# Performance work log

Hardware: AMD Instinct MI355X
Metric: run time of the kernel (lower is better)

## Reference

```python
import jax, jax.numpy as jnp
import numpy as np

D, H, W = 20, 18, 18      # f_dim = (20, 72//4, 72//4); depth == feature_ch
PI = 3.14159              # constant used in the torch module


def make_grid():
    # matches make_coordinate_grid_3d: normalized coords in [-1, 1]
    x = 2.0 * jnp.arange(W, dtype=jnp.float32) / (W - 1) - 1.0
    y = 2.0 * jnp.arange(H, dtype=jnp.float32) / (H - 1) - 1.0
    z = 2.0 * jnp.arange(D, dtype=jnp.float32) / (D - 1) - 1.0
    xx = jnp.broadcast_to(x[None, None, :], (D, H, W))
    yy = jnp.broadcast_to(y[None, :, None], (D, H, W))
    zz = jnp.broadcast_to(z[:, None, None], (D, H, W))
    grid_xy = jnp.stack([xx, yy], axis=-1)   # (D,H,W,2), order (x, y)
    return grid_xy, zz


def trilinear_sample(vol, grid):
    # vol: (D,H,W); grid: (D,H,W,3) with (x,y,z) in [-1,1]
    # F.grid_sample defaults: mode='bilinear' (trilinear), padding='zeros', align_corners=False
    ix = ((grid[..., 0] + 1.0) * W - 1.0) * 0.5
    iy = ((grid[..., 1] + 1.0) * H - 1.0) * 0.5
    iz = ((grid[..., 2] + 1.0) * D - 1.0) * 0.5
    x0, y0, z0 = jnp.floor(ix), jnp.floor(iy), jnp.floor(iz)
    wx, wy, wz = ix - x0, iy - y0, iz - z0
    vflat = vol.reshape(-1)
    out = jnp.zeros_like(ix)
    for cz in (0, 1):
        for cy in (0, 1):
            for cx in (0, 1):
                xi = x0 + cx
                yi = y0 + cy
                zi = z0 + cz
                w = ((wx if cx else 1.0 - wx)
                     * (wy if cy else 1.0 - wy)
                     * (wz if cz else 1.0 - wz))
                valid = ((xi >= 0) & (xi < W) & (yi >= 0) & (yi < H)
                         & (zi >= 0) & (zi < D))
                xi_c = jnp.clip(xi, 0, W - 1).astype(jnp.int32)
                yi_c = jnp.clip(yi, 0, H - 1).astype(jnp.int32)
                zi_c = jnp.clip(zi, 0, D - 1).astype(jnp.int32)
                idx = (zi_c * H + yi_c) * W + xi_c
                out = out + jnp.where(valid, w * vflat[idx], 0.0)
    return out


def setup_inputs() -> dict:
    key = jax.random.key(0)
    ks = jax.random.split(key, 10)
    B, P, F = 4096, 256, 20
    s = 0.05
    return {
        "feature_map": jax.random.normal(ks[0], (B, F, H, W), jnp.float32),
        "para_code": jax.random.normal(ks[1], (B, P), jnp.float32),
        "W1": jax.random.normal(ks[2], (P, P), jnp.float32) * s,
        "b1": jax.random.normal(ks[3], (P,), jnp.float32) * s,
        "Ws": jax.random.normal(ks[4], (P, F), jnp.float32) * s,
        "bs": jax.random.normal(ks[5], (F,), jnp.float32) * s,
        "Wr": jax.random.normal(ks[6], (P, F), jnp.float32) * s,
        "br": jax.random.normal(ks[7], (F,), jnp.float32) * s,
        "Wt": jax.random.normal(ks[8], (P, 2 * F), jnp.float32) * s,
        "bt": jax.random.normal(ks[9], (2 * F,), jnp.float32) * s,
    }


def reference(feature_map, para_code, W1, b1, Ws, bs, Wr, br, Wt, bt):
    B, F = feature_map.shape[0], feature_map.shape[1]  # F == D == 20
    grid_xy, grid_z = make_grid()
    h = jax.nn.relu(para_code @ W1 + b1)                     # commn_linear
    scale = jax.nn.sigmoid(h @ Ws + bs) * 2.0                # (B,F)
    angle = jnp.tanh(h @ Wr + br) * PI                       # (B,F)
    trans = jnp.tanh(h @ Wt + bt).reshape(B, F, 2)           # (B,F,2)
    c, s = jnp.cos(angle), jnp.sin(angle)
    rot = jnp.stack([jnp.stack([c, -s], -1),
                     jnp.stack([s, c], -1)], -2)             # (B,F,2,2)
    g = grid_xy.reshape(F, H * W, 2)                          # depth == feature_ch
    # per-channel affine: rotate, scale, translate each grid point
    tg = jnp.einsum('bfij,fpj->bfpi', rot, g)                 # (B,F,HW,2)
    tg = tg * scale[:, :, None, None] + trans[:, :, None, :]
    full_grid = jnp.concatenate(
        [tg.reshape(B, F, H, W, 2),
         jnp.broadcast_to(grid_z, (B, F, H, W))[..., None]], axis=-1)
    return jax.vmap(trilinear_sample)(feature_map, full_grid)
```

## Files before the change

### kernel.cpp

```cpp
#include <hip/hip_runtime.h>

#define PI_F 3.14159f

__global__ __launch_bounds__(256) void params_kernel(
    const float* __restrict__ pc, const float* __restrict__ W1, const float* __restrict__ b1,
    const float* __restrict__ Ws, const float* __restrict__ bs,
    const float* __restrict__ Wr, const float* __restrict__ br,
    const float* __restrict__ Wt, const float* __restrict__ bt,
    float* __restrict__ params)
{
    __shared__ float hbuf[4][260];
    __shared__ float raw[4][80];

    const int t    = threadIdx.x;
    const int lane = t & 63;
    const int b0   = blockIdx.x * 4;

    float pval[4][4];
    #pragma unroll
    for (int g = 0; g < 4; ++g)
        #pragma unroll
        for (int c = 0; c < 4; ++c)
            pval[g][c] = pc[(size_t)(b0 + g) * 256 + c * 64 + lane];

    float acc[4];
    #pragma unroll
    for (int g = 0; g < 4; ++g) acc[g] = b1[t];

    #pragma unroll
    for (int c = 0; c < 4; ++c) {
        for (int kk = 0; kk < 64; ++kk) {
            float w = W1[(c * 64 + kk) * 256 + t];
            #pragma unroll
            for (int g = 0; g < 4; ++g) {
                float pk = __int_as_float(
                    __builtin_amdgcn_readlane(__float_as_int(pval[g][c]), kk));
                acc[g] = fmaf(pk, w, acc[g]);
            }
        }
    }
    #pragma unroll
    for (int g = 0; g < 4; ++g) hbuf[g][t] = fmaxf(acc[g], 0.0f);
    __syncthreads();

    for (int task = t; task < 320; task += 256) {
        int g   = task / 80;
        int col = task - g * 80;
        const float* Wcol;
        float bias;
        int stride;
        if (col < 20)      { Wcol = Ws + col;        bias = bs[col];      stride = 20; }
        else if (col < 40) { Wcol = Wr + (col - 20); bias = br[col - 20]; stride = 20; }
        else               { Wcol = Wt + (col - 40); bias = bt[col - 40]; stride = 40; }
        const float4* h4 = (const float4*)hbuf[g];
        float a = bias;
        for (int k4 = 0; k4 < 64; ++k4) {
            float4 h = h4[k4];
            int k = k4 * 4;
            a = fmaf(h.x, Wcol[k * stride], a);
            a = fmaf(h.y, Wcol[(k + 1) * stride], a);
            a = fmaf(h.z, Wcol[(k + 2) * stride], a);
            a = fmaf(h.w, Wcol[(k + 3) * stride], a);
        }
        raw[g][col] = a;
    }
    __syncthreads();

    for (int task = t; task < 80; task += 256) {
        int g = task / 20;
        int f = task - g * 20;
        float sc  = 2.0f / (1.0f + expf(-raw[g][f]));
        float ang = PI_F * tanhf(raw[g][20 + f]);
        float tx  = tanhf(raw[g][40 + 2 * f]);
        float ty  = tanhf(raw[g][40 + 2 * f + 1]);
        float c = cosf(ang), s = sinf(ang);
        float* o = params + ((size_t)(b0 + g) * 20 + f) * 8;
        o[0] = 9.0f * sc * c;  o[1] = -9.0f * sc * s;  o[2] = fmaf(9.0f, tx, 9.5f);
        o[3] = 9.0f * sc * s;  o[4] =  9.0f * sc * c;  o[5] = fmaf(9.0f, ty, 9.5f);
        o[6] = 0.0f;           o[7] = 0.0f;
    }
}

__global__ __launch_bounds__(256, 8) void sample_kernel(
    const float* __restrict__ fmap, const float* __restrict__ params,
    float* __restrict__ out)
{
    __shared__ __align__(16) float lds[4][424];

    const int t    = threadIdx.x;
    const int lane = t & 63;
    const int w    = t >> 6;
    const int bid  = blockIdx.x;
    const int b    = bid / 5;
    const int c    = (bid - b * 5) * 4 + w;
    float* wv = lds[w];

    #pragma unroll
    for (int r = 0; r < 2; ++r) {
        int i = r * 64 + lane;
        if (i < 100) {
            int idx;
            if (i < 20)      idx = i;
            else if (i < 40) idx = 380 + (i - 20);
            else if (i < 76) {
                int q = i - 40;
                int y = 1 + (q < 18 ? q : q - 18);
                idx = y * 20 + (q < 18 ? 0 : 19);
            } else idx = 400 + (i - 76);
            wv[idx] = 0.0f;
        }
    }

    const float izf = (40.0f * (float)c - 19.0f) * (1.0f / 38.0f);
    const float fz0 = floorf(izf);
    const int   z0  = (int)fz0;
    const float wzB = izf - fz0;
    const bool  v0  = (z0 >= 0);
    const bool  v1  = (z0 + 1 <= 19);
    const float ew0 = v0 ? (1.0f - wzB) : 0.0f;
    const float ew1 = v1 ? wzB : 0.0f;
    const float* fb = fmap + (size_t)b * 6480;
    const float* s0 = fb + (v0 ? z0 : 0) * 324;
    const float* s1 = fb + (v1 ? z0 + 1 : 19) * 324;

    #pragma unroll
    for (int it = 0; it < 6; ++it) {
        int i = it * 64 + lane;
        if (i < 324) {
            float a  = s0[i];
            float bb = s1[i];
            int y = i / 18, x = i - y * 18;
            wv[(y + 1) * 20 + (x + 1)] = fmaf(a, ew0, bb * ew1);
        }
    }

    const float* pp = params + ((size_t)b * 20 + c) * 8;
    const float4 pA = *(const float4*)pp;
    const float2 pB = *(const float2*)(pp + 4);

    float* ob = out + (size_t)b * 6480 + c * 324;
    #pragma unroll
    for (int it = 0; it < 6; ++it) {
        int i = it * 64 + lane;
        if (i < 324) {
            int y = i / 18, x = i - y * 18;
            float X = (float)x * (2.0f / 17.0f) - 1.0f;
            float Y = (float)y * (2.0f / 17.0f) - 1.0f;
            float ix = fmaf(pA.x, X, fmaf(pA.y, Y, pA.z));
            float iy = fmaf(pA.w, X, fmaf(pB.x, Y, pB.y));
            ix = fminf(fmaxf(ix, 0.0f), 19.0f);
            iy = fminf(fmaxf(iy, 0.0f), 19.0f);
            float fx = floorf(ix), fy = floorf(iy);
            float u1 = ix - fx, vv = iy - fy;
            const float* s = wv + ((int)fy * 20 + (int)fx);
            float t00 = s[0], t01 = s[1], t10 = s[20], t11 = s[21];
            float u0 = 1.0f - u1, vc = 1.0f - vv;
            float r = fmaf(fmaf(t01, u1, t00 * u0), vc,
                           fmaf(t11, u1, t10 * u0) * vv);
            ob[i] = r;
        }
    }
}

extern "C" void kernel_launch(void* const* d_in, const int* in_sizes, int n_in,
                              void* d_out, int out_size, void* d_ws, size_t ws_size,
                              hipStream_t stream)
{
    const float* fmap = (const float*)d_in[0];
    const float* pc   = (const float*)d_in[1];
    const float* W1   = (const float*)d_in[2];
    const float* b1   = (const float*)d_in[3];
    const float* Ws   = (const float*)d_in[4];
    const float* bs   = (const float*)d_in[5];
    const float* Wr   = (const float*)d_in[6];
    const float* br   = (const float*)d_in[7];
    const float* Wt   = (const float*)d_in[8];
    const float* bt   = (const float*)d_in[9];
    float* out    = (float*)d_out;
    float* params = (float*)d_ws;

    const int B = in_sizes[0] / (20 * 18 * 18);

    params_kernel<<<B / 4, 256, 0, stream>>>(pc, W1, b1, Ws, bs, Wr, br, Wt, bt, params);
    sample_kernel<<<B * 5, 256, 0, stream>>>(fmap, params, out);
}
```

Measured before the change: 242.6 us.

## Batch 8 rows per params block and vectorize sampling with float2 and stride-21 LDS

The params kernel now handles 8 batch rows per block instead of 4, so each W1 load is reused across twice as many rows, and a couple of loops are unrolled. The sample kernel loads and stores float2 pairs, with each thread handling two adjacent pixels. The padded LDS tile row stride changes from 20 to 21, with the zero-border initialization rewritten to match. The params load is also hoisted above the tile fill. This trades more registers per thread and half as many params blocks for fewer memory instructions and better W1 reuse.

```diff
diff --git a/kernel.cpp b/kernel.cpp
--- a/kernel.cpp
+++ b/kernel.cpp
@@ -9,30 +9,31 @@
     const float* __restrict__ Wt, const float* __restrict__ bt,
     float* __restrict__ params)
 {
-    __shared__ float hbuf[4][260];
-    __shared__ float raw[4][80];
+    __shared__ float hbuf[8][260];
+    __shared__ float raw[8][80];
 
     const int t    = threadIdx.x;
     const int lane = t & 63;
-    const int b0   = blockIdx.x * 4;
-
-    float pval[4][4];
-    #pragma unroll
-    for (int g = 0; g < 4; ++g)
+    const int b0   = blockIdx.x * 8;
+
+    float pval[8][4];
+    #pragma unroll
+    for (int g = 0; g < 8; ++g)
         #pragma unroll
         for (int c = 0; c < 4; ++c)
             pval[g][c] = pc[(size_t)(b0 + g) * 256 + c * 64 + lane];
 
-    float acc[4];
-    #pragma unroll
-    for (int g = 0; g < 4; ++g) acc[g] = b1[t];
+    float acc[8];
+    #pragma unroll
+    for (int g = 0; g < 8; ++g) acc[g] = b1[t];
 
     #pragma unroll
     for (int c = 0; c < 4; ++c) {
+        #pragma unroll 4
         for (int kk = 0; kk < 64; ++kk) {
             float w = W1[(c * 64 + kk) * 256 + t];
             #pragma unroll
-            for (int g = 0; g < 4; ++g) {
+            for (int g = 0; g < 8; ++g) {
                 float pk = __int_as_float(
                     __builtin_amdgcn_readlane(__float_as_int(pval[g][c]), kk));
                 acc[g] = fmaf(pk, w, acc[g]);
@@ -40,10 +41,10 @@
         }
     }
     #pragma unroll
-    for (int g = 0; g < 4; ++g) hbuf[g][t] = fmaxf(acc[g], 0.0f);
+    for (int g = 0; g < 8; ++g) hbuf[g][t] = fmaxf(acc[g], 0.0f);
     __syncthreads();
 
-    for (int task = t; task < 320; task += 256) {
+    for (int task = t; task < 640; task += 256) {
         int g   = task / 80;
         int col = task - g * 80;
         const float* Wcol;
@@ -54,6 +55,7 @@
         else               { Wcol = Wt + (col - 40); bias = bt[col - 40]; stride = 40; }
         const float4* h4 = (const float4*)hbuf[g];
         float a = bias;
+        #pragma unroll 2
         for (int k4 = 0; k4 < 64; ++k4) {
             float4 h = h4[k4];
             int k = k4 * 4;
@@ -66,7 +68,7 @@
     }
     __syncthreads();
 
-    for (int task = t; task < 80; task += 256) {
+    for (int task = t; task < 160; task += 256) {
         int g = task / 20;
         int f = task - g * 20;
         float sc  = 2.0f / (1.0f + expf(-raw[g][f]));
@@ -85,7 +87,7 @@
     const float* __restrict__ fmap, const float* __restrict__ params,
     float* __restrict__ out)
 {
-    __shared__ __align__(16) float lds[4][424];
+    __shared__ __align__(16) float lds[4][448];
 
     const int t    = threadIdx.x;
     const int lane = t & 63;
@@ -95,19 +97,26 @@
     const int c    = (bid - b * 5) * 4 + w;
     float* wv = lds[w];
 
-    #pragma unroll
-    for (int r = 0; r < 2; ++r) {
-        int i = r * 64 + lane;
-        if (i < 100) {
-            int idx;
-            if (i < 20)      idx = i;
-            else if (i < 40) idx = 380 + (i - 20);
-            else if (i < 76) {
-                int q = i - 40;
-                int y = 1 + (q < 18 ? q : q - 18);
-                idx = y * 20 + (q < 18 ? 0 : 19);
-            } else idx = 400 + (i - 76);
-            wv[idx] = 0.0f;
+    const float* pp = params + ((size_t)b * 20 + c) * 8;
+    const float4 pA = *(const float4*)pp;
+    const float2 pB = *(const float2*)(pp + 4);
+
+    {
+        int i = lane;
+        int idx = (i < 21) ? i : 378 + i;
+        wv[idx] = 0.0f;
+        i = 64 + lane;
+        if (i < 124) {
+            int idx2;
+            if (i < 70) idx2 = 378 + i;
+            else {
+                int q = i - 70;
+                int y = 1 + q / 3;
+                int r = q - (q / 3) * 3;
+                int x = (r == 0) ? 0 : 18 + r;
+                idx2 = y * 21 + x;
+            }
+            wv[idx2] = 0.0f;
         }
     }
 
@@ -124,40 +133,45 @@
     const float* s1 = fb + (v1 ? z0 + 1 : 19) * 324;
 
     #pragma unroll
-    for (int it = 0; it < 6; ++it) {
-        int i = it * 64 + lane;
-        if (i < 324) {
-            float a  = s0[i];
-            float bb = s1[i];
-            int y = i / 18, x = i - y * 18;
-            wv[(y + 1) * 20 + (x + 1)] = fmaf(a, ew0, bb * ew1);
-        }
-    }
-
-    const float* pp = params + ((size_t)b * 20 + c) * 8;
-    const float4 pA = *(const float4*)pp;
-    const float2 pB = *(const float2*)(pp + 4);
+    for (int it = 0; it < 3; ++it) {
+        int k = it * 64 + lane;
+        if (k < 162) {
+            int i = 2 * k;
+            float2 a  = *(const float2*)(s0 + i);
+            float2 bb = *(const float2*)(s1 + i);
+            int y = k / 9;
+            int x = 2 * (k - y * 9);
+            int base = (y + 1) * 21 + (x + 1);
+            wv[base]     = fmaf(a.x, ew0, bb.x * ew1);
+            wv[base + 1] = fmaf(a.y, ew0, bb.y * ew1);
+        }
+    }
 
     float* ob = out + (size_t)b * 6480 + c * 324;
     #pragma unroll
-    for (int it = 0; it < 6; ++it) {
-        int i = it * 64 + lane;
-        if (i < 324) {
-            int y = i / 18, x = i - y * 18;
-            float X = (float)x * (2.0f / 17.0f) - 1.0f;
+    for (int it = 0; it < 3; ++it) {
+        int k = it * 64 + lane;
+        if (k < 162) {
+            int y  = k / 9;
+            int x0 = 2 * (k - y * 9);
             float Y = (float)y * (2.0f / 17.0f) - 1.0f;
-            float ix = fmaf(pA.x, X, fmaf(pA.y, Y, pA.z));
-            float iy = fmaf(pA.w, X, fmaf(pB.x, Y, pB.y));
-            ix = fminf(fmaxf(ix, 0.0f), 19.0f);
-            iy = fminf(fmaxf(iy, 0.0f), 19.0f);
-            float fx = floorf(ix), fy = floorf(iy);
-            float u1 = ix - fx, vv = iy - fy;
-            const float* s = wv + ((int)fy * 20 + (int)fx);
-            float t00 = s[0], t01 = s[1], t10 = s[20], t11 = s[21];
-            float u0 = 1.0f - u1, vc = 1.0f - vv;
-            float r = fmaf(fmaf(t01, u1, t00 * u0), vc,
-                           fmaf(t11, u1, t10 * u0) * vv);
-            ob[i] = r;
+            float r2[2];
+            #pragma unroll
+            for (int q = 0; q < 2; ++q) {
+                float X = (float)(x0 + q) * (2.0f / 17.0f) - 1.0f;
+                float ix = fmaf(pA.x, X, fmaf(pA.y, Y, pA.z));
+                float iy = fmaf(pA.w, X, fmaf(pB.x, Y, pB.y));
+                ix = fminf(fmaxf(ix, 0.0f), 19.0f);
+                iy = fminf(fmaxf(iy, 0.0f), 19.0f);
+                float fx = floorf(ix), fy = floorf(iy);
+                float u1 = ix - fx, vv = iy - fy;
+                const float* s = wv + ((int)fy * 21 + (int)fx);
+                float t00 = s[0], t01 = s[1], t10 = s[21], t11 = s[22];
+                float u0 = 1.0f - u1, vc = 1.0f - vv;
+                r2[q] = fmaf(fmaf(t01, u1, t00 * u0), vc,
+                             fmaf(t11, u1, t10 * u0) * vv);
+            }
+            *(float2*)(ob + y * 18 + x0) = make_float2(r2[0], r2[1]);
         }
     }
 }
@@ -181,6 +195,6 @@
 
     const int B = in_sizes[0] / (20 * 18 * 18);
 
-    params_kernel<<<B / 4, 256, 0, stream>>>(pc, W1, b1, Ws, bs, Wr, br, Wt, bt, params);
+    params_kernel<<<B / 8, 256, 0, stream>>>(pc, W1, b1, Ws, bs, Wr, br, Wt, bt, params);
     sample_kernel<<<B * 5, 256, 0, stream>>>(fmap, params, out);
 }
```

After: 256.2 us. +5.6%, slower.
